# Kernel optimization log

Hardware: AMD Instinct MI355X
Metric: run time of the kernel (lower is better)

The kernel has to match this reference:

```python
import jax, jax.numpy as jnp
import numpy as np

NUM_RBF = 16
RBF_D_MIN, RBF_D_MAX = 2.0, 22.0
CB_A, CB_B, CB_C = -0.58273431, 0.56802827, -0.54067466
TOP_K = 32
MAX_REL = 32
NPOS = 16
HID = 128
LN_EPS = 1e-5


def _gather_nodes(nodes, idx):
    # nodes: (B, L, D), idx: (B, L, K) -> (B, L, K, D)
    return jax.vmap(lambda n, i: n[i])(nodes, idx)


def _rbf_encode(D):
    mu = jnp.linspace(RBF_D_MIN, RBF_D_MAX, NUM_RBF, dtype=D.dtype)
    sigma = (RBF_D_MAX - RBF_D_MIN) / NUM_RBF
    return jnp.exp(-((D[..., None] - mu) ** 2) / (sigma ** 2))


def setup_inputs() -> dict:
    key = jax.random.key(0)
    ks = jax.random.split(key, 4)
    B, L = 2, 2048
    X = jax.random.normal(ks[0], (B, L, 4, 3), jnp.float32) * 10.0
    residue_mask = jnp.ones((B, L), jnp.float32)
    R_idx = jnp.arange(B * L, dtype=jnp.int32).reshape(B, L)
    chain_labels = jnp.zeros((B, L), jnp.int32)
    # learned params
    W_pos = jax.random.normal(ks[1], (NPOS, 2 * MAX_REL + 2), jnp.float32) * 0.05
    b_pos = jnp.zeros((NPOS,), jnp.float32)
    W_edge = jax.random.normal(ks[2], (HID, 25 * NUM_RBF + NPOS), jnp.float32) * 0.02
    ln_gamma = jnp.ones((HID,), jnp.float32)
    ln_beta = jnp.zeros((HID,), jnp.float32)
    return {"X": X, "residue_mask": residue_mask, "R_idx": R_idx,
            "chain_labels": chain_labels, "W_pos": W_pos, "b_pos": b_pos,
            "W_edge": W_edge, "ln_gamma": ln_gamma, "ln_beta": ln_beta}


def reference(X, residue_mask, R_idx, chain_labels, W_pos, b_pos, W_edge, ln_gamma, ln_beta):
    B, L = X.shape[0], X.shape[1]
    K = min(TOP_K, L)
    # virtual CB from backbone N, CA, C
    N, CA, C = X[..., 0, :], X[..., 1, :], X[..., 2, :]
    b = CA - N
    c = C - CA
    a = jnp.cross(b, c, axis=-1)
    CB = (CB_A * a + CB_B * b + CB_C * c + CA)[..., None, :]
    atoms_5 = jnp.concatenate([X, CB], axis=-2)  # (B, L, 5, 3)
    # kNN on CA coords with invalid residues pushed far away
    diff = CA[:, :, None, :] - CA[:, None, :, :]
    dist_sq = jnp.sum(diff * diff, axis=-1)  # (B, L, L)
    inv_mask = 1.0 - residue_mask
    dist_sq = dist_sq + inv_mask[:, None, :] * 1e6
    _, E_idx = jax.lax.top_k(-dist_sq, K)  # smallest-k indices, (B, L, K)
    # gather neighbor 5-atom coords and compute 25 pairwise distances
    Xf = atoms_5.reshape(B, L, 15)
    Xg = _gather_nodes(Xf, E_idx).reshape(B, L, K, 5, 3)
    d2 = jnp.sum((atoms_5[:, :, None, :, None, :] - Xg[:, :, :, None, :, :]) ** 2, axis=-1)
    D = jnp.sqrt(d2 + 1e-6)  # (B, L, K, 5, 5)
    rbf = _rbf_encode(D).reshape(B, L, K, 25 * NUM_RBF)
    # positional encodings (standard ProteinMPNN form)
    Rg = _gather_nodes(R_idx[..., None], E_idx)[..., 0]  # (B, L, K)
    Cg = _gather_nodes(chain_labels[..., None], E_idx)[..., 0]
    d_rel = Rg - R_idx[:, :, None]
    same_chain = (Cg == chain_labels[:, :, None])
    d_clip = jnp.clip(d_rel + MAX_REL, 0, 2 * MAX_REL)
    d_final = jnp.where(same_chain, d_clip, 2 * MAX_REL + 1)
    oh = jax.nn.one_hot(d_final, 2 * MAX_REL + 2, dtype=rbf.dtype)
    pos_enc = jnp.einsum('blkc,pc->blkp', oh, W_pos) + b_pos
    # edge embedding + layernorm
    edge_input = jnp.concatenate([pos_enc, rbf], axis=-1)  # (B, L, K, 416)
    h = jnp.einsum('blkf,hf->blkh', edge_input, W_edge)
    mean = jnp.mean(h, axis=-1, keepdims=True)
    var = jnp.var(h, axis=-1, keepdims=True)
    E = (h - mean) * jax.lax.rsqrt(var + LN_EPS) * ln_gamma + ln_beta
    return E_idx, E
```

## Files before the change

kernel.cpp:

```cpp
#include <hip/hip_runtime.h>
#include <hip/hip_bf16.h>

#define LEN   2048
#define KNB   32
#define HID   128
#define FS    512

typedef unsigned long long ull;
typedef unsigned int uint32;
typedef float f32x4 __attribute__((ext_vector_type(4)));

__device__ __forceinline__ void bar_lgkm() {
    asm volatile("s_waitcnt lgkmcnt(0)" ::: "memory");
    __builtin_amdgcn_s_barrier();
    asm volatile("" ::: "memory");
}

__global__ __launch_bounds__(256) void prep_kernel(
    const float* __restrict__ X, const float* __restrict__ mask,
    const float* __restrict__ W_edge,
    float4* __restrict__ CAm, int* __restrict__ Wf8) {
    const int t = blockIdx.x * 256 + threadIdx.x;
    if (t < 2 * LEN) {
        const float* p = X + (size_t)t * 12;
        CAm[t] = make_float4(p[3], p[4], p[5],
                             __fmul_rn(__fsub_rn(1.0f, mask[t]), 1000000.0f));
    }
    if (t < 13312) {
        const float4 w = ((const float4*)W_edge)[t];
        int r = __builtin_amdgcn_cvt_pk_fp8_f32(w.x, w.y, 0, false);
        r = __builtin_amdgcn_cvt_pk_fp8_f32(w.z, w.w, r, true);
        Wf8[t] = r;
    }
}

__global__ __launch_bounds__(256) void topk_kernel(
    const float4* __restrict__ CAm, float* __restrict__ eidx_out) {
    const int row = blockIdx.x;
    const int b = row >> 11;
    const int i = row & (LEN - 1);
    const int tid = threadIdx.x;

    __shared__ int hist[512];
    __shared__ ull cand[LEN];
    __shared__ int candcnt;
    __shared__ int selB;

    const float4* C = CAm + (size_t)b * LEN;
    const float4 ci = C[i];

    uint32 d2b[8];
#pragma unroll
    for (int q = 0; q < 8; ++q) {
        const float4 cj = C[q * 256 + tid];
        float dx = __fsub_rn(ci.x, cj.x);
        float dy = __fsub_rn(ci.y, cj.y);
        float dz = __fsub_rn(ci.z, cj.z);
        float d2 = __fadd_rn(__fadd_rn(__fmul_rn(dx, dx), __fmul_rn(dy, dy)),
                             __fmul_rn(dz, dz));
        d2 = __fadd_rn(d2, cj.w);
        d2b[q] = __float_as_uint(d2);
    }

    hist[tid] = 0; hist[tid + 256] = 0;
    if (tid == 0) candcnt = 0;
    __syncthreads();
#pragma unroll
    for (int q = 0; q < 8; ++q) atomicAdd(&hist[d2b[q] >> 22], 1);
    __syncthreads();

    if (tid < 64) {
        int loc[8];
        int s = 0;
#pragma unroll
        for (int t = 0; t < 8; ++t) { loc[t] = hist[tid * 8 + t]; s += loc[t]; }
        int incl = s;
#pragma unroll
        for (int off = 1; off < 64; off <<= 1) {
            int o = __shfl_up(incl, off, 64);
            if (tid >= off) incl += o;
        }
        const int excl = incl - s;
        if (excl < KNB && incl >= KNB) {
            int c = excl;
#pragma unroll
            for (int t = 0; t < 8; ++t) {
                int c2 = c + loc[t];
                if (c < KNB && c2 >= KNB) selB = tid * 8 + t;
                c = c2;
            }
        }
    }
    __syncthreads();
    const uint32 B = (uint32)selB;

#pragma unroll
    for (int q = 0; q < 8; ++q) {
        if ((d2b[q] >> 22) <= B) {
            int p = atomicAdd(&candcnt, 1);
            cand[p] = (((ull)d2b[q]) << 32) | (uint32)(q * 256 + tid);
        }
    }
    __syncthreads();
    const int M = candcnt;

    for (int c = tid; c < M; c += 256) {
        const ull k = cand[c];
        int r = 0;
        for (int m = 0; m < M; ++m) r += (cand[m] < k);
        if (r < KNB)
            eidx_out[(size_t)row * KNB + r] = (float)(uint32)(k & 0xFFFFFFFFull);
    }
}

__device__ __forceinline__ void load_res_atoms(const float* __restrict__ p, float* dst) {
    const float Nx = p[0], Ny = p[1], Nz = p[2];
    const float Ax = p[3], Ay = p[4], Az = p[5];
    const float Cx = p[6], Cy = p[7], Cz = p[8];
    const float Ox = p[9], Oy = p[10], Oz = p[11];
    const float bx = Ax - Nx, by = Ay - Ny, bz = Az - Nz;
    const float cx = Cx - Ax, cy = Cy - Ay, cz = Cz - Az;
    const float axv = by * cz - bz * cy;
    const float ayv = bz * cx - bx * cz;
    const float azv = bx * cy - by * cx;
    dst[0] = Nx;  dst[1] = Ny;  dst[2] = Nz;
    dst[3] = Ax;  dst[4] = Ay;  dst[5] = Az;
    dst[6] = Cx;  dst[7] = Cy;  dst[8] = Cz;
    dst[9] = Ox;  dst[10] = Oy; dst[11] = Oz;
    dst[12] = -0.58273431f * axv + 0.56802827f * bx + -0.54067466f * cx + Ax;
    dst[13] = -0.58273431f * ayv + 0.56802827f * by + -0.54067466f * cy + Ay;
    dst[14] = -0.58273431f * azv + 0.56802827f * bz + -0.54067466f * cz + Az;
}

__device__ __forceinline__ int pk4(float a, float b, float c, float d) {
    int r = __builtin_amdgcn_cvt_pk_fp8_f32(a, b, 0, false);
    return __builtin_amdgcn_cvt_pk_fp8_f32(c, d, r, true);
}

#define E1  3.2053337e-1f
#define E3  3.2931300e-2f
#define E5  3.3834001e-3f
#define E7  3.4760500e-4f

__device__ __forceinline__ void compute_features(
    int tid, int Ri, int Ci,
    const float* __restrict__ wposL,
    const int* jR, const int* jC,
    const float (*natoms)[15], const float* iatoms,
    unsigned char* featF8) {
    {
        const int e = tid >> 4, p = tid & 15;
        const int drel = jR[e] - Ri;
        const int same = (jC[e] == Ci);
        int dc = drel + 32;
        dc = dc < 0 ? 0 : (dc > 64 ? 64 : dc);
        const int df = same ? dc : 65;
        const float v = wposL[p * 66 + df];
        const int pb = __builtin_amdgcn_cvt_pk_fp8_f32(v, 0.0f, 0, false);
        featF8[e * FS + ((e & 7) << 4) + p] = (unsigned char)(pb & 0xFF);
    }
#pragma unroll
    for (int it = 0; it < 2; ++it) {
        const int task = tid + it * 512;
        if (task < 800) {
            const int mn = task >> 5, e = task & 31;
            const int m = mn / 5, n = mn - m * 5;
            const float ax = iatoms[m * 3 + 0];
            const float ay = iatoms[m * 3 + 1];
            const float az = iatoms[m * 3 + 2];
            const float* na = &natoms[e][n * 3];
            const float dx = ax - na[0], dy = ay - na[1], dz = az - na[2];
            const float D = sqrtf(dx * dx + dy * dy + dz * dz + 1e-6f);
            const float Dc = fminf(D, 40.0f);
            const float v4 = Dc - 7.3333333f;
            const float A4  = __expf(-0.64f * v4 * v4);
            const float C4  = __expf(1.7066667f * v4);
            const float Ci4 = 1.0f / C4;
            int4 w4;
            {
                const float f3 = A4 * Ci4 * E1;
                const float f2 = f3 * Ci4 * E3;
                const float f1 = f2 * Ci4 * E5;
                const float f0 = f1 * Ci4 * E7;
                w4.x = pk4(f0, f1, f2, f3);
            }
            {
                const float f5 = A4 * C4 * E1;
                const float f6 = f5 * C4 * E3;
                const float f7 = f6 * C4 * E5;
                w4.y = pk4(A4, f5, f6, f7);
            }
            const float v12 = Dc - 18.0f;
            const float A12  = __expf(-0.64f * v12 * v12);
            const float C12  = C4 * 1.24140e-8f;
            const float Ci12 = Ci4 * 8.05543e7f;
            {
                const float f11 = A12 * Ci12 * E1;
                const float f10 = f11 * Ci12 * E3;
                const float f9  = f10 * Ci12 * E5;
                const float f8  = f9  * Ci12 * E7;
                w4.z = pk4(f8, f9, f10, f11);
            }
            {
                const float f13 = A12 * C12 * E1;
                const float f14 = f13 * C12 * E3;
                const float f15 = f14 * C12 * E5;
                w4.w = pk4(A12, f13, f14, f15);
            }
            *(int4*)(featF8 + e * FS + (((1 + mn) ^ (e & 7)) << 4)) = w4;
        }
    }
}

__global__ __launch_bounds__(512, 6) void edge_kernel(
    const float* __restrict__ X,
    const int* __restrict__ Ridx, const int* __restrict__ Chain,
    const float* __restrict__ W_pos, const float* __restrict__ b_pos,
    const unsigned char* __restrict__ Wf8,
    const float* __restrict__ lng, const float* __restrict__ lnb,
    const float* __restrict__ eidx_f, float* __restrict__ outE) {
    const int tid = threadIdx.x;
    const int row0 = blockIdx.x * 4;
    const int b = row0 >> 11;
    const int i0 = row0 & (LEN - 1);

    __shared__ __align__(16) unsigned char featF8[32 * FS];
    __shared__ __align__(16) float hbuf[32 * 132];
    __shared__ float natoms[4][32][15];
    __shared__ float iatoms[4][16];
    __shared__ float wposL[16 * 66];
    __shared__ int jR[4][KNB], jC[4][KNB];
    __shared__ int riS[4], ciS[4];

    const float* Xb = X + (size_t)b * LEN * 12;

    const int w = tid >> 6, l = tid & 63, lr = l & 15, lg = l >> 4;
    long wreg[13];
    {
        const unsigned char* wb = Wf8 + (size_t)(w * 16 + lr) * 416 + lg * 8;
#pragma unroll
        for (int ks = 0; ks < 13; ++ks)
            wreg[ks] = *(const long*)(wb + ks * 32);
    }

    for (int t = tid; t < 1056; t += 512)
        wposL[t] = W_pos[t] + b_pos[t / 66];
    if (tid < 128) {
        const int r = tid >> 5, e = tid & 31;
        const int j = (int)eidx_f[(size_t)(row0 + r) * KNB + e];
        jR[r][e] = Ridx[b * LEN + j];
        jC[r][e] = Chain[b * LEN + j];
        load_res_atoms(Xb + j * 12, &natoms[r][e][0]);
    } else if (tid < 132) {
        const int r = tid - 128;
        load_res_atoms(Xb + (size_t)(i0 + r) * 12, &iatoms[r][0]);
    } else if (tid < 136) {
        riS[tid - 132] = Ridx[b * LEN + i0 + (tid - 132)];
    } else if (tid < 140) {
        ciS[tid - 136] = Chain[b * LEN + i0 + (tid - 136)];
    }
    bar_lgkm();

    compute_features(tid, riS[0], ciS[0], wposL,
                     jR[0], jC[0], natoms[0], iatoms[0], featF8);
    bar_lgkm();

    for (int r = 0; r < 4; ++r) {
        const int row = row0 + r;

        f32x4 acc0 = {0.f, 0.f, 0.f, 0.f}, acc1 = acc0;
        {
            const int sw = lr & 7;
            const int mb = lg >> 1;
            const unsigned char* fb0 = featF8 + lr * FS + (lg & 1) * 8;
            const unsigned char* fb1 = featF8 + (16 + lr) * FS + (lg & 1) * 8;
#pragma unroll
            for (int ks = 0; ks < 13; ++ks) {
                const int moff = ((2 * ks + mb) ^ sw) << 4;
                const long a0 = *(const long*)(fb0 + moff);
                const long a1 = *(const long*)(fb1 + moff);
                acc0 = __builtin_amdgcn_mfma_f32_16x16x32_fp8_fp8(a0, wreg[ks], acc0, 0, 0, 0);
                acc1 = __builtin_amdgcn_mfma_f32_16x16x32_fp8_fp8(a1, wreg[ks], acc1, 0, 0, 0);
            }
        }
#pragma unroll
        for (int rr = 0; rr < 4; ++rr) {
            hbuf[(lg * 4 + rr) * 132 + w * 16 + lr]      = acc0[rr];
            hbuf[(16 + lg * 4 + rr) * 132 + w * 16 + lr] = acc1[rr];
        }
        bar_lgkm();

        {
            const int g = tid >> 4, l2 = tid & 15;
            const float4* hb4 = (const float4*)(hbuf + g * 132 + l2 * 8);
            const float4 v0 = hb4[0], v1 = hb4[1];
            float s = v0.x + v0.y + v0.z + v0.w + v1.x + v1.y + v1.z + v1.w;
            float ssq = v0.x * v0.x + v0.y * v0.y + v0.z * v0.z + v0.w * v0.w
                      + v1.x * v1.x + v1.y * v1.y + v1.z * v1.z + v1.w * v1.w;
#pragma unroll
            for (int off = 1; off < 16; off <<= 1) {
                s += __shfl_xor(s, off, 64);
                ssq += __shfl_xor(ssq, off, 64);
            }
            const float mean = s * (1.0f / 128.0f);
            const float rstd = rsqrtf(ssq * (1.0f / 128.0f) - mean * mean + 1e-5f);

            float4* ob = (float4*)(outE + ((size_t)row * KNB + g) * HID + l2 * 8);
            const float4 g0 = *(const float4*)(lng + l2 * 8);
            const float4 g1 = *(const float4*)(lng + l2 * 8 + 4);
            const float4 b0 = *(const float4*)(lnb + l2 * 8);
            const float4 b1 = *(const float4*)(lnb + l2 * 8 + 4);
            float4 o0, o1;
            o0.x = (v0.x - mean) * rstd * g0.x + b0.x;
            o0.y = (v0.y - mean) * rstd * g0.y + b0.y;
            o0.z = (v0.z - mean) * rstd * g0.z + b0.z;
            o0.w = (v0.w - mean) * rstd * g0.w + b0.w;
            o1.x = (v1.x - mean) * rstd * g1.x + b1.x;
            o1.y = (v1.y - mean) * rstd * g1.y + b1.y;
            o1.z = (v1.z - mean) * rstd * g1.z + b1.z;
            o1.w = (v1.w - mean) * rstd * g1.w + b1.w;
            ob[0] = o0;
            ob[1] = o1;
        }
        if (r < 3) {
            compute_features(tid, riS[r + 1], ciS[r + 1], wposL,
                             jR[r + 1], jC[r + 1], natoms[r + 1], iatoms[r + 1],
                             featF8);
        }
        bar_lgkm();
    }
}

extern "C" void kernel_launch(void* const* d_in, const int* in_sizes, int n_in,
                              void* d_out, int out_size, void* d_ws, size_t ws_size,
                              hipStream_t stream) {
    const float* X      = (const float*)d_in[0];
    const float* mask   = (const float*)d_in[1];
    const int*   Ridx   = (const int*)d_in[2];
    const int*   Chain  = (const int*)d_in[3];
    const float* W_pos  = (const float*)d_in[4];
    const float* b_pos  = (const float*)d_in[5];
    const float* W_edge = (const float*)d_in[6];
    const float* lng    = (const float*)d_in[7];
    const float* lnb    = (const float*)d_in[8];

    float* out  = (float*)d_out;
    float* eidx = out;
    float* E    = out + (size_t)2 * LEN * KNB;

    float4* CAm = (float4*)d_ws;
    unsigned char* Wf8 = (unsigned char*)d_ws + 2 * LEN * 16;

    const int nrow = 2 * LEN;
    prep_kernel<<<52, 256, 0, stream>>>(X, mask, W_edge, CAm, (int*)Wf8);
    topk_kernel<<<nrow, 256, 0, stream>>>(CAm, eidx);
    edge_kernel<<<nrow / 4, 512, 0, stream>>>(X, Ridx, Chain, W_pos, b_pos, Wf8,
                                              lng, lnb, eidx, E);
}
```

Measured before the change: 62.06 us.

## Process two rows per iteration in edge kernel with bf16 staging buffer

Each edge-kernel block now handles 8 rows instead of 4, processing two rows per loop iteration with double feature buffers. This halves the barriers per row, amortises the W_edge register load over more rows, and gives more independent MFMA chains between syncs. The GEMM result staged in LDS is stored as bf16 instead of fp32 to keep shared memory in bounds, at some cost in LayerNorm input precision. Occupancy hint drops from 6 to 4 and the grid is halved.

```diff
diff --git a/kernel.cpp b/kernel.cpp
--- a/kernel.cpp
+++ b/kernel.cpp
@@ -9,6 +9,7 @@
 typedef unsigned long long ull;
 typedef unsigned int uint32;
 typedef float f32x4 __attribute__((ext_vector_type(4)));
+typedef __bf16 bf16x8v __attribute__((ext_vector_type(8)));
 
 __device__ __forceinline__ void bar_lgkm() {
     asm volatile("s_waitcnt lgkmcnt(0)" ::: "memory");
@@ -212,7 +213,61 @@
     }
 }
 
-__global__ __launch_bounds__(512, 6) void edge_kernel(
+__device__ __forceinline__ void gemm_row(
+    const unsigned char* feat, const long* wreg, int lr, int lg,
+    f32x4& acc0, f32x4& acc1) {
+    const int sw = lr & 7;
+    const int mb = lg >> 1;
+    const unsigned char* fb0 = feat + lr * FS + (lg & 1) * 8;
+    const unsigned char* fb1 = feat + (16 + lr) * FS + (lg & 1) * 8;
+#pragma unroll
+    for (int ks = 0; ks < 13; ++ks) {
+        const int moff = ((2 * ks + mb) ^ sw) << 4;
+        const long a0 = *(const long*)(fb0 + moff);
+        const long a1 = *(const long*)(fb1 + moff);
+        acc0 = __builtin_amdgcn_mfma_f32_16x16x32_fp8_fp8(a0, wreg[ks], acc0, 0, 0, 0);
+        acc1 = __builtin_amdgcn_mfma_f32_16x16x32_fp8_fp8(a1, wreg[ks], acc1, 0, 0, 0);
+    }
+}
+
+__device__ __forceinline__ void ln_store(
+    const __bf16* hb, int row, int tid,
+    const float* __restrict__ lng, const float* __restrict__ lnb,
+    float* __restrict__ outE) {
+    const int g = tid >> 4, l2 = tid & 15;
+    const bf16x8v hv = *(const bf16x8v*)(hb + g * 132 + l2 * 8);
+    float v[8];
+#pragma unroll
+    for (int k = 0; k < 8; ++k) v[k] = (float)hv[k];
+    float s = 0.f, ssq = 0.f;
+#pragma unroll
+    for (int k = 0; k < 8; ++k) { s += v[k]; ssq += v[k] * v[k]; }
+#pragma unroll
+    for (int off = 1; off < 16; off <<= 1) {
+        s += __shfl_xor(s, off, 64);
+        ssq += __shfl_xor(ssq, off, 64);
+    }
+    const float mean = s * (1.0f / 128.0f);
+    const float rstd = rsqrtf(ssq * (1.0f / 128.0f) - mean * mean + 1e-5f);
+    float4* ob = (float4*)(outE + ((size_t)row * KNB + g) * HID + l2 * 8);
+    const float4 g0 = *(const float4*)(lng + l2 * 8);
+    const float4 g1 = *(const float4*)(lng + l2 * 8 + 4);
+    const float4 b0 = *(const float4*)(lnb + l2 * 8);
+    const float4 b1 = *(const float4*)(lnb + l2 * 8 + 4);
+    float4 o0, o1;
+    o0.x = (v[0] - mean) * rstd * g0.x + b0.x;
+    o0.y = (v[1] - mean) * rstd * g0.y + b0.y;
+    o0.z = (v[2] - mean) * rstd * g0.z + b0.z;
+    o0.w = (v[3] - mean) * rstd * g0.w + b0.w;
+    o1.x = (v[4] - mean) * rstd * g1.x + b1.x;
+    o1.y = (v[5] - mean) * rstd * g1.y + b1.y;
+    o1.z = (v[6] - mean) * rstd * g1.z + b1.z;
+    o1.w = (v[7] - mean) * rstd * g1.w + b1.w;
+    ob[0] = o0;
+    ob[1] = o1;
+}
+
+__global__ __launch_bounds__(512, 4) void edge_kernel(
     const float* __restrict__ X,
     const int* __restrict__ Ridx, const int* __restrict__ Chain,
     const float* __restrict__ W_pos, const float* __restrict__ b_pos,
@@ -220,17 +275,18 @@
     const float* __restrict__ lng, const float* __restrict__ lnb,
     const float* __restrict__ eidx_f, float* __restrict__ outE) {
     const int tid = threadIdx.x;
-    const int row0 = blockIdx.x * 4;
+    const int row0 = blockIdx.x * 8;
     const int b = row0 >> 11;
     const int i0 = row0 & (LEN - 1);
 
-    __shared__ __align__(16) unsigned char featF8[32 * FS];
-    __shared__ __align__(16) float hbuf[32 * 132];
-    __shared__ float natoms[4][32][15];
-    __shared__ float iatoms[4][16];
+    __shared__ __align__(16) unsigned char featF8[2][32 * FS];
+    __shared__ __align__(16) __bf16 hbA[32 * 132];
+    __shared__ __align__(16) __bf16 hbB[32 * 132];
+    __shared__ float natoms[8][32][15];
+    __shared__ float iatoms[8][16];
     __shared__ float wposL[16 * 66];
-    __shared__ int jR[4][KNB], jC[4][KNB];
-    __shared__ int riS[4], ciS[4];
+    __shared__ int jR[8][KNB], jC[8][KNB];
+    __shared__ int riS[8], ciS[8];
 
     const float* Xb = X + (size_t)b * LEN * 12;
 
@@ -245,87 +301,53 @@
 
     for (int t = tid; t < 1056; t += 512)
         wposL[t] = W_pos[t] + b_pos[t / 66];
-    if (tid < 128) {
+    if (tid < 256) {
         const int r = tid >> 5, e = tid & 31;
         const int j = (int)eidx_f[(size_t)(row0 + r) * KNB + e];
         jR[r][e] = Ridx[b * LEN + j];
         jC[r][e] = Chain[b * LEN + j];
         load_res_atoms(Xb + j * 12, &natoms[r][e][0]);
-    } else if (tid < 132) {
-        const int r = tid - 128;
+    } else if (tid < 264) {
+        const int r = tid - 256;
         load_res_atoms(Xb + (size_t)(i0 + r) * 12, &iatoms[r][0]);
-    } else if (tid < 136) {
-        riS[tid - 132] = Ridx[b * LEN + i0 + (tid - 132)];
-    } else if (tid < 140) {
-        ciS[tid - 136] = Chain[b * LEN + i0 + (tid - 136)];
+    } else if (tid < 272) {
+        riS[tid - 264] = Ridx[b * LEN + i0 + (tid - 264)];
+    } else if (tid < 280) {
+        ciS[tid - 272] = Chain[b * LEN + i0 + (tid - 272)];
     }
     bar_lgkm();
 
-    compute_features(tid, riS[0], ciS[0], wposL,
-                     jR[0], jC[0], natoms[0], iatoms[0], featF8);
+    compute_features(tid, riS[0], ciS[0], wposL, jR[0], jC[0],
+                     natoms[0], iatoms[0], featF8[0]);
+    compute_features(tid, riS[1], ciS[1], wposL, jR[1], jC[1],
+                     natoms[1], iatoms[1], featF8[1]);
     bar_lgkm();
 
-    for (int r = 0; r < 4; ++r) {
-        const int row = row0 + r;
-
-        f32x4 acc0 = {0.f, 0.f, 0.f, 0.f}, acc1 = acc0;
-        {
-            const int sw = lr & 7;
-            const int mb = lg >> 1;
-            const unsigned char* fb0 = featF8 + lr * FS + (lg & 1) * 8;
-            const unsigned char* fb1 = featF8 + (16 + lr) * FS + (lg & 1) * 8;
-#pragma unroll
-            for (int ks = 0; ks < 13; ++ks) {
-                const int moff = ((2 * ks + mb) ^ sw) << 4;
-                const long a0 = *(const long*)(fb0 + moff);
-                const long a1 = *(const long*)(fb1 + moff);
-                acc0 = __builtin_amdgcn_mfma_f32_16x16x32_fp8_fp8(a0, wreg[ks], acc0, 0, 0, 0);
-                acc1 = __builtin_amdgcn_mfma_f32_16x16x32_fp8_fp8(a1, wreg[ks], acc1, 0, 0, 0);
-            }
-        }
+    for (int it = 0; it < 4; ++it) {
+        const int ra = row0 + 2 * it, rb = ra + 1;
+
+        f32x4 accA0 = {0.f, 0.f, 0.f, 0.f}, accA1 = accA0;
+        f32x4 accB0 = accA0, accB1 = accA0;
+        gemm_row(featF8[0], wreg, lr, lg, accA0, accA1);
+        gemm_row(featF8[1], wreg, lr, lg, accB0, accB1);
 #pragma unroll
         for (int rr = 0; rr < 4; ++rr) {
-            hbuf[(lg * 4 + rr) * 132 + w * 16 + lr]      = acc0[rr];
-            hbuf[(16 + lg * 4 + rr) * 132 + w * 16 + lr] = acc1[rr];
+            const int ch = w * 16 + lr;
+            hbA[(lg * 4 + rr) * 132 + ch]      = (__bf16)accA0[rr];
+            hbA[(16 + lg * 4 + rr) * 132 + ch] = (__bf16)accA1[rr];
+            hbB[(lg * 4 + rr) * 132 + ch]      = (__bf16)accB0[rr];
+            hbB[(16 + lg * 4 + rr) * 132 + ch] = (__bf16)accB1[rr];
         }
         bar_lgkm();
 
-        {
-            const int g = tid >> 4, l2 = tid & 15;
-            const float4* hb4 = (const float4*)(hbuf + g * 132 + l2 * 8);
-            const float4 v0 = hb4[0], v1 = hb4[1];
-            float s = v0.x + v0.y + v0.z + v0.w + v1.x + v1.y + v1.z + v1.w;
-            float ssq = v0.x * v0.x + v0.y * v0.y + v0.z * v0.z + v0.w * v0.w
-                      + v1.x * v1.x + v1.y * v1.y + v1.z * v1.z + v1.w * v1.w;
-#pragma unroll
-            for (int off = 1; off < 16; off <<= 1) {
-                s += __shfl_xor(s, off, 64);
-                ssq += __shfl_xor(ssq, off, 64);
-            }
-            const float mean = s * (1.0f / 128.0f);
-            const float rstd = rsqrtf(ssq * (1.0f / 128.0f) - mean * mean + 1e-5f);
-
-            float4* ob = (float4*)(outE + ((size_t)row * KNB + g) * HID + l2 * 8);
-            const float4 g0 = *(const float4*)(lng + l2 * 8);
-            const float4 g1 = *(const float4*)(lng + l2 * 8 + 4);
-            const float4 b0 = *(const float4*)(lnb + l2 * 8);
-            const float4 b1 = *(const float4*)(lnb + l2 * 8 + 4);
-            float4 o0, o1;
-            o0.x = (v0.x - mean) * rstd * g0.x + b0.x;
-            o0.y = (v0.y - mean) * rstd * g0.y + b0.y;
-            o0.z = (v0.z - mean) * rstd * g0.z + b0.z;
-            o0.w = (v0.w - mean) * rstd * g0.w + b0.w;
-            o1.x = (v1.x - mean) * rstd * g1.x + b1.x;
-            o1.y = (v1.y - mean) * rstd * g1.y + b1.y;
-            o1.z = (v1.z - mean) * rstd * g1.z + b1.z;
-            o1.w = (v1.w - mean) * rstd * g1.w + b1.w;
-            ob[0] = o0;
-            ob[1] = o1;
-        }
-        if (r < 3) {
-            compute_features(tid, riS[r + 1], ciS[r + 1], wposL,
-                             jR[r + 1], jC[r + 1], natoms[r + 1], iatoms[r + 1],
-                             featF8);
+        ln_store(hbA, ra, tid, lng, lnb, outE);
+        ln_store(hbB, rb, tid, lng, lnb, outE);
+        if (it < 3) {
+            const int na = 2 * it + 2, nb = 2 * it + 3;
+            compute_features(tid, riS[na], ciS[na], wposL, jR[na], jC[na],
+                             natoms[na], iatoms[na], featF8[0]);
+            compute_features(tid, riS[nb], ciS[nb], wposL, jR[nb], jC[nb],
+                             natoms[nb], iatoms[nb], featF8[1]);
         }
         bar_lgkm();
     }
@@ -354,6 +376,6 @@
     const int nrow = 2 * LEN;
     prep_kernel<<<52, 256, 0, stream>>>(X, mask, W_edge, CAm, (int*)Wf8);
     topk_kernel<<<nrow, 256, 0, stream>>>(CAm, eidx);
-    edge_kernel<<<nrow / 4, 512, 0, stream>>>(X, Ridx, Chain, W_pos, b_pos, Wf8,
+    edge_kernel<<<nrow / 8, 512, 0, stream>>>(X, Ridx, Chain, W_pos, b_pos, Wf8,
                                               lng, lnb, eidx, E);
 }
```

New measurement: 62.23 us. Within noise of the previous version (+0.3%).
